# Performance work log

Measured on AMD Instinct MI355X. Metric: run time of the kernel, lower is better.

Reference implementation:

```python
import jax, jax.numpy as jnp
import numpy as np
from jax import lax

B, C, T = 16, 32, 512
GAF_SIZE = 128
LATENT = 128
EPS = 1e-8


def _conv(x, w, b, stride):
    # x: (N, Cin, H, W), w: (Cout, Cin, kh, kw)
    y = lax.conv_general_dilated(x, w, (stride, stride), 'SAME',
                                 dimension_numbers=('NCHW', 'OIHW', 'NCHW'))
    return jax.nn.relu(y + b[None, :, None, None])


def _compute_gaf(x_raw):
    # x_raw: (B, C, T) -> (B*C, 2, S, S) with channels [GASF, GADF]
    S = GAF_SIZE
    # Piecewise Aggregate Approximation: T -> S
    x = x_raw.reshape(B, C, S, T // S).mean(axis=-1)        # (B, C, S)
    # Min-max normalize each series to [-1, 1]
    mn = x.min(axis=-1, keepdims=True)
    mx = x.max(axis=-1, keepdims=True)
    x = jnp.clip(2.0 * (x - mn) / (mx - mn + EPS) - 1.0, -1.0, 1.0)
    # phi = arccos(x); use trig identities to avoid explicit arccos
    sq = jnp.sqrt(jnp.clip(1.0 - x * x, 0.0, 1.0))          # sin(phi)
    xi, xj = x[..., :, None], x[..., None, :]
    si, sj = sq[..., :, None], sq[..., None, :]
    gasf = xi * xj - si * sj                                 # cos(phi_i + phi_j)
    gadf = si * xj - xi * sj                                 # sin(phi_i - phi_j)
    gaf = jnp.stack([gasf, gadf], axis=2)                    # (B, C, 2, S, S)
    return gaf.reshape(B * C, 2, S, S).astype(jnp.float32)


def _encoder(gaf, W1, b1, W2, b2, W3, b3, W4, b4, Wfc, bfc):
    h = _conv(gaf, W1, b1, 2)   # (B*C, 32, 64, 64)
    h = _conv(h, W2, b2, 2)     # (B*C, 64, 32, 32)
    h = _conv(h, W3, b3, 2)     # (B*C, 128, 16, 16)
    h = _conv(h, W4, b4, 2)     # (B*C, 256, 8, 8)
    h = h.mean(axis=(2, 3))     # global average pool -> (B*C, 256)
    return h @ Wfc + bfc        # (B*C, LATENT)


def setup_inputs() -> dict:
    key = jax.random.key(0)
    ks = jax.random.split(key, 12)
    p = lambda k, shp: (jax.random.normal(k, shp, dtype=jnp.float32) * 0.05)
    return {
        'x_raw': jax.random.normal(ks[0], (B, C, T), dtype=jnp.float32),
        'W1': p(ks[1], (32, 2, 3, 3)),   'b1': jnp.zeros((32,), jnp.float32),
        'W2': p(ks[2], (64, 32, 3, 3)),  'b2': jnp.zeros((64,), jnp.float32),
        'W3': p(ks[3], (128, 64, 3, 3)), 'b3': jnp.zeros((128,), jnp.float32),
        'W4': p(ks[4], (256, 128, 3, 3)),'b4': jnp.zeros((256,), jnp.float32),
        'Wfc': p(ks[5], (256, LATENT)),  'bfc': jnp.zeros((LATENT,), jnp.float32),
    }


def reference(x_raw, W1, b1, W2, b2, W3, b3, W4, b4, Wfc, bfc):
    # GAF computed from detached raw EEG in the original (numpy CPU path)
    gaf = lax.stop_gradient(_compute_gaf(x_raw))
    z = _encoder(gaf, W1, b1, W2, b2, W3, b3, W4, b4, Wfc, bfc)
    return z.reshape(B, C, LATENT).mean(axis=1)              # (B, LATENT)
```

## Files before the change

### kernel.cpp

```cpp
#include <hip/hip_runtime.h>
#include <hip/hip_bf16.h>

#define DEV __device__ __forceinline__

constexpr int kB = 16, kC = 32, kT = 512, kS = 128, kBC = 512, kLatent = 128;
constexpr float kEps = 1e-8f;

using bf16 = __hip_bfloat16;
using bf16x8 = __attribute__((ext_vector_type(8))) short;
using f32x4  = __attribute__((ext_vector_type(4))) float;

DEV unsigned short f2bf(float v) {
    bf16 h = __float2bfloat16(v);
    return *(unsigned short*)&h;
}

DEV void gld16(const void* g, void* l) {
    __builtin_amdgcn_global_load_lds(
        (const __attribute__((address_space(1))) unsigned*)g,
        (__attribute__((address_space(3))) unsigned*)l, 16, 0, 0);
}

__global__ void gaf_stats_kernel(const float* __restrict__ x_raw,
                                 float* __restrict__ xn, float* __restrict__ sq) {
    int bc = blockIdx.x;
    int s  = threadIdx.x;
    const float* xp = x_raw + (size_t)bc * kT;
    float v = 0.25f * (xp[4*s] + xp[4*s+1] + xp[4*s+2] + xp[4*s+3]);
    __shared__ float smn[kS], smx[kS];
    smn[s] = v; smx[s] = v;
    __syncthreads();
    for (int off = kS/2; off > 0; off >>= 1) {
        if (s < off) {
            smn[s] = fminf(smn[s], smn[s+off]);
            smx[s] = fmaxf(smx[s], smx[s+off]);
        }
        __syncthreads();
    }
    float mn = smn[0], mx = smx[0];
    float xv = 2.0f * (v - mn) / (mx - mn + kEps) - 1.0f;
    xv = fminf(fmaxf(xv, -1.0f), 1.0f);
    float sv = sqrtf(fminf(fmaxf(1.0f - xv*xv, 0.0f), 1.0f));
    xn[bc*kS + s] = xv;
    sq[bc*kS + s] = sv;
}

__global__ void wtrans_all_kernel(const float* __restrict__ w1,
                                  const float* __restrict__ w2,
                                  const float* __restrict__ w3,
                                  const float* __restrict__ w4,
                                  bf16* __restrict__ w1b, bf16* __restrict__ wt2,
                                  bf16* __restrict__ wt3, bf16* __restrict__ wt4) {
    int idx = blockIdx.x * blockDim.x + threadIdx.x;
    if (idx < 1024) {
        int oc = idx >> 5, k = idx & 31;
        w1b[idx] = __float2bfloat16(k < 18 ? w1[oc*18 + k] : 0.0f);
        return;
    }
    idx -= 1024;
    const float* src; bf16* dst; int CIN, COUT;
    if (idx < 18432)       { src = w2; dst = wt2; CIN = 32;  COUT = 64;  }
    else if (idx < 92160)  { idx -= 18432;  src = w3; dst = wt3; CIN = 64;  COUT = 128; }
    else if (idx < 387072) { idx -= 92160;  src = w4; dst = wt4; CIN = 128; COUT = 256; }
    else return;
    int ic = idx % CIN;
    int oc = (idx / CIN) % COUT;
    int t  = idx / (CIN * COUT);
    dst[((size_t)t * COUT + oc) * CIN + ic] = __float2bfloat16(src[((size_t)oc * CIN + ic) * 9 + t]);
}

__global__ __launch_bounds__(256, 2)
void conv12_kernel(const float* __restrict__ xn, const float* __restrict__ sq,
                   const bf16* __restrict__ w1b, const float* __restrict__ b1,
                   const bf16* __restrict__ wt2, const float* __restrict__ b2,
                   bf16* __restrict__ out, int img0) {
    __shared__ float xl[kS], sl[kS];
    __shared__ __align__(16) union { short G[576][40]; short H[2][288][40]; } U;
    __shared__ __align__(16) short Bs2[3][64][32];
    __shared__ __align__(16) short W1s[32][40];

    int tid  = threadIdx.x;
    int lane = tid & 63;
    int wv   = tid >> 6;
    int mblk = blockIdx.x;
    int bz   = blockIdx.y;
    int bc   = img0 + bz;

    gld16((const char*)wt2 + 0*4096 + tid*16, (char*)Bs2 + 0*4096 + tid*16);
    gld16((const char*)wt2 + 1*4096 + tid*16, (char*)Bs2 + 1*4096 + tid*16);

    if (tid < 128) {
        xl[tid] = xn[(size_t)bc * kS + tid];
        int rr = tid >> 2, sg = tid & 3;
        *(uint4*)&W1s[rr][sg*8] = *(const uint4*)(w1b + rr*32 + sg*8);
    } else {
        sl[tid - 128] = sq[(size_t)bc * kS + (tid - 128)];
    }
    __syncthreads();

    #pragma unroll
    for (int it = 0; it < 3; ++it) {
        int idx = it * 256 + tid;
        if (idx >= 576) break;
        int trow = idx >> 6, hx = idx & 63;
        int iy = 8 * mblk + trow;
        unsigned int pk[16];
        #pragma unroll
        for (int j = 0; j < 16; ++j) pk[j] = 0u;
        if (iy < 64) {
            float xr[3], sr[3], xc[3], sc[3];
            #pragma unroll
            for (int k = 0; k < 3; ++k) {
                int iyy = 2*iy + k, ixx = 2*hx + k;
                bool vy = iyy < kS, vx = ixx < kS;
                xr[k] = vy ? xl[iyy] : 0.0f;  sr[k] = vy ? sl[iyy] : 0.0f;
                xc[k] = vx ? xl[ixx] : 0.0f;  sc[k] = vx ? sl[ixx] : 0.0f;
            }
            unsigned short gs[18];
            #pragma unroll
            for (int ky = 0; ky < 3; ++ky)
                #pragma unroll
                for (int kx = 0; kx < 3; ++kx) {
                    gs[ky*3+kx]   = f2bf(xr[ky]*xc[kx] - sr[ky]*sc[kx]);
                    gs[9+ky*3+kx] = f2bf(sr[ky]*xc[kx] - xr[ky]*sc[kx]);
                }
            #pragma unroll
            for (int j = 0; j < 9; ++j)
                pk[j] = (unsigned int)gs[2*j] | ((unsigned int)gs[2*j+1] << 16);
        }
        #pragma unroll
        for (int j = 0; j < 4; ++j) *(uint4*)&U.G[idx][j*8] = ((uint4*)pk)[j];
    }
    __syncthreads();

    f32x4 c1[9][2];
    bf16x8 w1f0 = *(const bf16x8*)&W1s[(lane & 15)][(lane>>4)*8];
    bf16x8 w1f1 = *(const bf16x8*)&W1s[16 + (lane & 15)][(lane>>4)*8];
    #pragma unroll
    for (int j = 0; j < 9; ++j) {
        int mt = 4*j + wv;
        bf16x8 af = *(const bf16x8*)&U.G[mt*16 + (lane & 15)][(lane>>4)*8];
        f32x4 zz = f32x4{0.f, 0.f, 0.f, 0.f};
        c1[j][0] = __builtin_amdgcn_mfma_f32_16x16x32_bf16(af, w1f0, zz, 0, 0, 0);
        c1[j][1] = __builtin_amdgcn_mfma_f32_16x16x32_bf16(af, w1f1, zz, 0, 0, 0);
    }
    __syncthreads();

    #pragma unroll
    for (int j = 0; j < 9; ++j) {
        int mt = 4*j + wv;
        #pragma unroll
        for (int h = 0; h < 2; ++h) {
            int oc = h*16 + (lane & 15);
            float bb = b1[oc];
            #pragma unroll
            for (int rg = 0; rg < 4; ++rg) {
                int pos = mt*16 + (lane>>4)*4 + rg;
                int trow = pos >> 6, hx = pos & 63;
                float v = fmaxf(c1[j][h][rg] + bb, 0.0f);
                if (8*mblk + trow >= 64) v = 0.0f;
                U.H[hx & 1][trow*32 + (hx >> 1)][oc] = (short)f2bf(v);
            }
        }
    }
    __syncthreads();

    f32x4 acc[2][4];
    #pragma unroll
    for (int i = 0; i < 2; ++i)
        #pragma unroll
        for (int j = 0; j < 4; ++j) acc[i][j] = f32x4{0.f, 0.f, 0.f, 0.f};

    for (int tap = 0; tap < 9; ++tap) {
        if (tap + 2 < 9)
            gld16((const char*)wt2 + (tap+2)*4096 + tid*16,
                  (char*)Bs2 + ((tap+2)%3)*4096 + tid*16);
        int ky = tap / 3, kx = tap % 3;
        int trow = 2*wv + ky;
        const short* bsl = &Bs2[tap%3][0][0];
        bf16x8 af[2], bfr[4];
        #pragma unroll
        for (int mi = 0; mi < 2; ++mi) {
            int ocol = mi*16 + (lane & 15);
            int x = 2*ocol + kx;
            bf16x8 z = {0,0,0,0,0,0,0,0};
            af[mi] = (x < 64) ? *(const bf16x8*)&U.H[kx & 1][trow*32 + (x>>1)][(lane>>4)*8] : z;
        }
        #pragma unroll
        for (int ni = 0; ni < 4; ++ni)
            bfr[ni] = *(const bf16x8*)&bsl[(ni*16 + (lane&15))*32 + (lane>>4)*8];
        #pragma unroll
        for (int mi = 0; mi < 2; ++mi)
            #pragma unroll
            for (int ni = 0; ni < 4; ++ni)
                acc[mi][ni] = __builtin_amdgcn_mfma_f32_16x16x32_bf16(af[mi], bfr[ni], acc[mi][ni], 0, 0, 0);
        __syncthreads();
    }

    int oy = 4*mblk + wv;
    #pragma unroll
    for (int ni = 0; ni < 4; ++ni) {
        int oc = ni*16 + (lane & 15);
        float b = b2[oc];
        #pragma unroll
        for (int mi = 0; mi < 2; ++mi)
            #pragma unroll
            for (int rg = 0; rg < 4; ++rg) {
                int ocol = 16*mi + (lane>>4)*4 + rg;
                float v = fmaxf(acc[mi][ni][rg] + b, 0.0f);
                out[(((size_t)bz*32 + oy)*32 + ocol)*64 + oc] = __float2bfloat16(v);
            }
    }
}

__global__ __launch_bounds__(256)
void conv34_kernel(const bf16* __restrict__ h2, const bf16* __restrict__ wt3,
                   const float* __restrict__ b3, const bf16* __restrict__ wt4,
                   const float* __restrict__ b4, float* __restrict__ pooled,
                   int img0, const bf16* __restrict__ zbuf) {
    __shared__ __align__(16) short H3[257*128];
    __shared__ __align__(16) short stA[2*256*32];
    __shared__ __align__(16) short stB[2*128*32];

    int tid  = threadIdx.x;
    int lane = tid & 63;
    int wv   = tid >> 6;
    int img  = blockIdx.x;

    if (tid < 128) H3[256*128 + tid] = 0;

    auto issue1 = [&](int s, int buf) {
        int tap = s >> 1, icb = (s & 1) * 32;
        int ky = tap / 3, kx = tap % 3;
        #pragma unroll
        for (int j = 0; j < 4; ++j) {
            int row = wv*64 + j*16 + (lane >> 2);
            int oy = row >> 4, ox = row & 15;
            int iy = 2*oy + ky, ix = 2*ox + kx;
            const bf16* src = (iy < 32 && ix < 32)
                ? h2 + (((size_t)img*32 + iy)*32 + ix)*64 + icb + (lane & 3)*8
                : zbuf + (lane & 3)*8;
            gld16(src, (char*)&stA[buf*8192 + (wv*64 + j*16)*32] + lane*16);
        }
        #pragma unroll
        for (int j = 0; j < 2; ++j) {
            int brow = wv*32 + j*16 + (lane >> 2);
            const bf16* src = wt3 + ((size_t)tap*128 + brow)*64 + icb + (lane & 3)*8;
            gld16(src, (char*)&stB[buf*4096 + (wv*32 + j*16)*32] + lane*16);
        }
    };

    f32x4 acc[4][8];
    #pragma unroll
    for (int i = 0; i < 4; ++i)
        #pragma unroll
        for (int j = 0; j < 8; ++j) acc[i][j] = f32x4{0.f, 0.f, 0.f, 0.f};

    issue1(0, 0);
    __syncthreads();

    for (int s = 0; s < 18; ++s) {
        int cur = s & 1;
        if (s + 1 < 18) issue1(s + 1, cur ^ 1);
        bf16x8 af[4];
        #pragma unroll
        for (int mi = 0; mi < 4; ++mi)
            af[mi] = *(const bf16x8*)&stA[cur*8192 + (wv*64 + mi*16 + (lane&15))*32 + (lane>>4)*8];
        #pragma unroll
        for (int ni = 0; ni < 8; ++ni) {
            bf16x8 bfr = *(const bf16x8*)&stB[cur*4096 + (ni*16 + (lane&15))*32 + (lane>>4)*8];
            #pragma unroll
            for (int mi = 0; mi < 4; ++mi)
                acc[mi][ni] = __builtin_amdgcn_mfma_f32_16x16x32_bf16(af[mi], bfr, acc[mi][ni], 0, 0, 0);
        }
        __syncthreads();
    }

    #pragma unroll
    for (int ni = 0; ni < 8; ++ni) {
        int oc = ni*16 + (lane & 15);
        float bb = b3[oc];
        int q = oc >> 3, ql = oc & 7;
        #pragma unroll
        for (int mi = 0; mi < 4; ++mi)
            #pragma unroll
            for (int rg = 0; rg < 4; ++rg) {
                int pos = wv*64 + mi*16 + (lane>>4)*4 + rg;
                float v = fmaxf(acc[mi][ni][rg] + bb, 0.0f);
                H3[pos*128 + (q ^ ((pos>>1)&7))*8 + ql] = (short)f2bf(v);
            }
    }

    auto issue2 = [&](int s, int buf) {
        int tap = s >> 2, icb = (s & 3) * 32;
        #pragma unroll
        for (int j = 0; j < 4; ++j) {
            int brow = wv*64 + j*16 + (lane >> 2);
            const bf16* src = wt4 + ((size_t)tap*256 + brow)*128 + icb + (lane & 3)*8;
            gld16(src, (char*)&stA[buf*8192 + (wv*64 + j*16)*32] + lane*16);
        }
    };

    issue2(0, 0);
    __syncthreads();

    f32x4 ac4[4][4];
    #pragma unroll
    for (int i = 0; i < 4; ++i)
        #pragma unroll
        for (int j = 0; j < 4; ++j) ac4[i][j] = f32x4{0.f, 0.f, 0.f, 0.f};

    for (int s = 0; s < 36; ++s) {
        int cur = s & 1;
        if (s + 1 < 36) issue2(s + 1, cur ^ 1);
        int tap = s >> 2, kq0 = (s & 3) * 4 + (lane >> 4);
        int ky = tap / 3, kx = tap % 3;
        bf16x8 af[4];
        #pragma unroll
        for (int mi = 0; mi < 4; ++mi) {
            int m = mi*16 + (lane & 15);
            int oy = m >> 3, ox = m & 7;
            int iy = 2*oy + ky, ix = 2*ox + kx;
            int pos = (iy < 16 && ix < 16) ? iy*16 + ix : 256;
            af[mi] = *(const bf16x8*)&H3[pos*128 + (kq0 ^ ((pos>>1)&7))*8];
        }
        #pragma unroll
        for (int ni = 0; ni < 4; ++ni) {
            bf16x8 bfr = *(const bf16x8*)&stA[cur*8192 + (wv*64 + ni*16 + (lane&15))*32 + (lane>>4)*8];
            #pragma unroll
            for (int mi = 0; mi < 4; ++mi)
                ac4[mi][ni] = __builtin_amdgcn_mfma_f32_16x16x32_bf16(af[mi], bfr, ac4[mi][ni], 0, 0, 0);
        }
        __syncthreads();
    }

    #pragma unroll
    for (int ni = 0; ni < 4; ++ni) {
        int oc = wv*64 + ni*16 + (lane & 15);
        float bb = b4[oc];
        float ssum = 0.0f;
        #pragma unroll
        for (int mi = 0; mi < 4; ++mi)
            #pragma unroll
            for (int rg = 0; rg < 4; ++rg) ssum += fmaxf(ac4[mi][ni][rg] + bb, 0.0f);
        ssum += __shfl_xor(ssum, 16);
        ssum += __shfl_xor(ssum, 32);
        if (lane < 16)
            pooled[((size_t)(img0 + img))*256 + wv*64 + ni*16 + lane] = ssum * (1.0f/64.0f);
    }
}

__global__ void poolfc_kernel(const float* __restrict__ pooled, const float* __restrict__ Wfc,
                              const float* __restrict__ bfc, float* __restrict__ out) {
    int b = blockIdx.x;
    int t = threadIdx.x;
    __shared__ float pm[256];
    #pragma unroll
    for (int q = 0; q < 2; ++q) {
        int k = q*128 + t;
        float s = 0.0f;
        #pragma unroll
        for (int c = 0; c < kC; ++c) s += pooled[((size_t)(b*kC + c))*256 + k];
        pm[k] = s * (1.0f/kC);
    }
    __syncthreads();
    float acc = bfc[t];
    for (int k = 0; k < 256; ++k) acc = fmaf(pm[k], Wfc[(size_t)k*kLatent + t], acc);
    out[(size_t)b*kLatent + t] = acc;
}

extern "C" void kernel_launch(void* const* d_in, const int* in_sizes, int n_in,
                              void* d_out, int out_size, void* d_ws, size_t ws_size,
                              hipStream_t stream) {
    const float* x_raw = (const float*)d_in[0];
    const float* W1 = (const float*)d_in[1];  const float* b1 = (const float*)d_in[2];
    const float* W2 = (const float*)d_in[3];  const float* b2 = (const float*)d_in[4];
    const float* W3 = (const float*)d_in[5];  const float* b3 = (const float*)d_in[6];
    const float* W4 = (const float*)d_in[7];  const float* b4 = (const float*)d_in[8];
    const float* Wfc = (const float*)d_in[9]; const float* bfc = (const float*)d_in[10];
    float* out = (float*)d_out;

    char* wsb = (char*)d_ws;
    float* xn     = (float*)(wsb);
    float* sq     = (float*)(wsb + (256u<<10));
    float* pooled = (float*)(wsb + (512u<<10));
    bf16* Wt2     = (bf16*)(wsb + (1280u<<10));
    bf16* Wt3     = (bf16*)(wsb + (1316u<<10));
    bf16* Wt4     = (bf16*)(wsb + (1460u<<10));
    bf16* W1b     = (bf16*)(wsb + (2036u<<10));
    bf16* zbuf    = (bf16*)(wsb + (2040u<<10));
    char* chunk_base = wsb + (2048u<<10);

    const size_t perImg = 32u*32u*64u*2u;
    int chunk = 4;
    for (int c = 512; c >= 4; c >>= 1) {
        if ((2048u<<10) + (size_t)c * perImg <= ws_size) { chunk = c; break; }
    }

    hipMemsetAsync(zbuf, 0, 1024, stream);
    gaf_stats_kernel<<<kBC, kS, 0, stream>>>(x_raw, xn, sq);
    wtrans_all_kernel<<<(388096 + 255)/256, 256, 0, stream>>>(W1, W2, W3, W4, W1b, Wt2, Wt3, Wt4);

    for (int img0 = 0; img0 < kBC; img0 += chunk) {
        int nimg = chunk;
        bf16* h2 = (bf16*)chunk_base;

        conv12_kernel<<<dim3(8, nimg), 256, 0, stream>>>(xn, sq, W1b, b1, Wt2, b2, h2, img0);
        conv34_kernel<<<nimg, 256, 0, stream>>>(h2, Wt3, b3, Wt4, b4, pooled, img0, zbuf);
    }

    poolfc_kernel<<<kB, kLatent, 0, stream>>>(pooled, Wfc, bfc, out);
}
```

Before: 244.4 us.

## Split fused conv3/conv4 kernel into separate kernels with global h3 buffer

Replaces the single per-image conv3+conv4 kernel with two kernels: conv3 runs two blocks per image (each covering half the output rows) and writes a swizzled, parity-split h3 to global memory, and conv4 loads that h3 into LDS. Conv3 now stages the whole input half-tile in LDS once and register-prefetches weights instead of async double-buffered im2col loads. This raises parallelism and occupancy (launch bounds 2 blocks/SM, smaller LDS per block) at the cost of an extra global round trip for h3 and an additional kernel launch per chunk.

```diff
diff --git a/kernel.cpp b/kernel.cpp
--- a/kernel.cpp
+++ b/kernel.cpp
@@ -213,140 +213,192 @@
     }
 }
 
-__global__ __launch_bounds__(256)
-void conv34_kernel(const bf16* __restrict__ h2, const bf16* __restrict__ wt3,
-                   const float* __restrict__ b3, const bf16* __restrict__ wt4,
-                   const float* __restrict__ b4, float* __restrict__ pooled,
-                   int img0, const bf16* __restrict__ zbuf) {
-    __shared__ __align__(16) short H3[257*128];
-    __shared__ __align__(16) short stA[2*256*32];
-    __shared__ __align__(16) short stB[2*128*32];
+__global__ __launch_bounds__(256, 2)
+void conv3_kernel(const bf16* __restrict__ h2, const bf16* __restrict__ wt3,
+                  const float* __restrict__ b3, bf16* __restrict__ h3g) {
+    __shared__ __align__(16) short T[34816];
+    __shared__ __align__(16) short Bs[4096];
 
     int tid  = threadIdx.x;
     int lane = tid & 63;
     int wv   = tid >> 6;
+    int half = blockIdx.x;
+    int img  = blockIdx.y;
+    const bf16* h2i = h2 + (size_t)img * 65536;
+
+    for (int it = 0; it < 17; ++it) {
+        int o = it*256 + tid;
+        int r = o >> 8, c = o & 255;
+        int ix = c >> 3, icq = c & 7;
+        int gr = half*16 + r;
+        uint4 v = {0u,0u,0u,0u};
+        if (gr < 32) v = *(const uint4*)(h2i + gr*2048 + ix*64 + icq*8);
+        int dst = ((((ix&1)*17 + r)*16 + (ix>>1))*8 + (icq ^ ((ix>>1)&7)))*8;
+        *(uint4*)&T[dst] = v;
+    }
+    int brow = tid >> 1, bseg = tid & 1;
+    {
+        const bf16* p = wt3 + (size_t)brow*64 + bseg*16;
+        uint4 v0 = *(const uint4*)p, v1 = *(const uint4*)(p + 8);
+        *(uint4*)&Bs[brow*32 + bseg*16]     = v0;
+        *(uint4*)&Bs[brow*32 + bseg*16 + 8] = v1;
+    }
+    __syncthreads();
+
+    f32x4 acc[2][8];
+    #pragma unroll
+    for (int i = 0; i < 2; ++i)
+        #pragma unroll
+        for (int j = 0; j < 8; ++j) acc[i][j] = f32x4{0.f,0.f,0.f,0.f};
+
+    for (int s = 0; s < 18; ++s) {
+        uint4 nb0, nb1;
+        if (s + 1 < 18) {
+            int tapn = (s+1) >> 1, icbn = ((s+1) & 1) * 32;
+            const bf16* p = wt3 + ((size_t)tapn*128 + brow)*64 + icbn + bseg*16;
+            nb0 = *(const uint4*)p; nb1 = *(const uint4*)(p + 8);
+        }
+        int tap = s >> 1, icq0 = (s & 1) * 4;
+        int ky = tap / 3, kx = tap % 3;
+        bf16x8 af[2], bfr[8];
+        #pragma unroll
+        for (int mi = 0; mi < 2; ++mi) {
+            int m = wv*32 + mi*16 + (lane & 15);
+            int oyL = m >> 4, ox3 = m & 15;
+            int iy = 2*oyL + ky, ix = 2*ox3 + kx;
+            int par = ix & 1, colx = ix >> 1;
+            int colc = colx > 15 ? 15 : colx;
+            int addr = (((par*17 + iy)*16 + colc)*8 + ((icq0 + (lane>>4)) ^ (colc & 7)))*8;
+            bf16x8 v = *(const bf16x8*)&T[addr];
+            bf16x8 z = {0,0,0,0,0,0,0,0};
+            af[mi] = (ix < 32) ? v : z;
+        }
+        #pragma unroll
+        for (int ni = 0; ni < 8; ++ni)
+            bfr[ni] = *(const bf16x8*)&Bs[(ni*16 + (lane&15))*32 + (lane>>4)*8];
+        #pragma unroll
+        for (int mi = 0; mi < 2; ++mi)
+            #pragma unroll
+            for (int ni = 0; ni < 8; ++ni)
+                acc[mi][ni] = __builtin_amdgcn_mfma_f32_16x16x32_bf16(af[mi], bfr[ni], acc[mi][ni], 0, 0, 0);
+        __syncthreads();
+        if (s + 1 < 18) {
+            *(uint4*)&Bs[brow*32 + bseg*16]     = nb0;
+            *(uint4*)&Bs[brow*32 + bseg*16 + 8] = nb1;
+            __syncthreads();
+        }
+    }
+
+    bf16* h3o = h3g + (size_t)img * 32768;
+    #pragma unroll
+    for (int ni = 0; ni < 8; ++ni) {
+        int oc3 = ni*16 + (lane & 15);
+        float bb = b3[oc3];
+        int kq = oc3 >> 3, ql = oc3 & 7;
+        #pragma unroll
+        for (int mi = 0; mi < 2; ++mi)
+            #pragma unroll
+            for (int rg = 0; rg < 4; ++rg) {
+                int m = wv*32 + mi*16 + (lane>>4)*4 + rg;
+                int oyL = m >> 4, ox3 = m & 15;
+                int iy4 = half*8 + oyL;
+                int par = ox3 & 1, col4 = ox3 >> 1;
+                int slot = kq ^ col4;
+                int off = ((par*16 + iy4)*8 + col4)*128 + slot*8 + ql;
+                float v = fmaxf(acc[mi][ni][rg] + bb, 0.0f);
+                h3o[off] = __float2bfloat16(v);
+            }
+    }
+}
+
+__global__ __launch_bounds__(256, 2)
+void conv4_kernel(const bf16* __restrict__ h3g, const bf16* __restrict__ wt4,
+                  const float* __restrict__ b4, float* __restrict__ pooled,
+                  int img0) {
+    __shared__ __align__(16) short H3s[32768];
+    __shared__ __align__(16) short Bs[8192];
+
+    int tid  = threadIdx.x;
+    int lane = tid & 63;
+    int wn   = tid >> 6;
     int img  = blockIdx.x;
 
-    if (tid < 128) H3[256*128 + tid] = 0;
-
-    auto issue1 = [&](int s, int buf) {
-        int tap = s >> 1, icb = (s & 1) * 32;
+    const char* h3b = (const char*)(h3g + (size_t)img * 32768);
+    #pragma unroll
+    for (int it = 0; it < 16; ++it)
+        gld16(h3b + (it*256 + tid)*16, (char*)H3s + (it*256 + tid)*16);
+
+    uint4 vb[4];
+    {
+        const bf16* p = wt4 + (size_t)tid * 128;
+        #pragma unroll
+        for (int j = 0; j < 4; ++j) vb[j] = *(const uint4*)(p + j*8);
+        #pragma unroll
+        for (int j = 0; j < 4; ++j) *(uint4*)&Bs[tid*32 + j*8] = vb[j];
+    }
+    __syncthreads();
+
+    f32x4 acc[4][4];
+    #pragma unroll
+    for (int i = 0; i < 4; ++i)
+        #pragma unroll
+        for (int j = 0; j < 4; ++j) acc[i][j] = f32x4{0.f,0.f,0.f,0.f};
+
+    for (int s = 0; s < 36; ++s) {
+        uint4 nb[4];
+        if (s + 1 < 36) {
+            int tapn = (s+1) >> 2, icbn = ((s+1) & 3) * 32;
+            const bf16* p = wt4 + ((size_t)tapn*256 + tid)*128 + icbn;
+            #pragma unroll
+            for (int j = 0; j < 4; ++j) nb[j] = *(const uint4*)(p + j*8);
+        }
+        int tap = s >> 2;
         int ky = tap / 3, kx = tap % 3;
-        #pragma unroll
-        for (int j = 0; j < 4; ++j) {
-            int row = wv*64 + j*16 + (lane >> 2);
-            int oy = row >> 4, ox = row & 15;
-            int iy = 2*oy + ky, ix = 2*ox + kx;
-            const bf16* src = (iy < 32 && ix < 32)
-                ? h2 + (((size_t)img*32 + iy)*32 + ix)*64 + icb + (lane & 3)*8
-                : zbuf + (lane & 3)*8;
-            gld16(src, (char*)&stA[buf*8192 + (wv*64 + j*16)*32] + lane*16);
-        }
-        #pragma unroll
-        for (int j = 0; j < 2; ++j) {
-            int brow = wv*32 + j*16 + (lane >> 2);
-            const bf16* src = wt3 + ((size_t)tap*128 + brow)*64 + icb + (lane & 3)*8;
-            gld16(src, (char*)&stB[buf*4096 + (wv*32 + j*16)*32] + lane*16);
-        }
-    };
-
-    f32x4 acc[4][8];
-    #pragma unroll
-    for (int i = 0; i < 4; ++i)
-        #pragma unroll
-        for (int j = 0; j < 8; ++j) acc[i][j] = f32x4{0.f, 0.f, 0.f, 0.f};
-
-    issue1(0, 0);
-    __syncthreads();
-
-    for (int s = 0; s < 18; ++s) {
-        int cur = s & 1;
-        if (s + 1 < 18) issue1(s + 1, cur ^ 1);
-        bf16x8 af[4];
-        #pragma unroll
-        for (int mi = 0; mi < 4; ++mi)
-            af[mi] = *(const bf16x8*)&stA[cur*8192 + (wv*64 + mi*16 + (lane&15))*32 + (lane>>4)*8];
-        #pragma unroll
-        for (int ni = 0; ni < 8; ++ni) {
-            bf16x8 bfr = *(const bf16x8*)&stB[cur*4096 + (ni*16 + (lane&15))*32 + (lane>>4)*8];
-            #pragma unroll
-            for (int mi = 0; mi < 4; ++mi)
-                acc[mi][ni] = __builtin_amdgcn_mfma_f32_16x16x32_bf16(af[mi], bfr, acc[mi][ni], 0, 0, 0);
-        }
-        __syncthreads();
-    }
-
-    #pragma unroll
-    for (int ni = 0; ni < 8; ++ni) {
-        int oc = ni*16 + (lane & 15);
-        float bb = b3[oc];
-        int q = oc >> 3, ql = oc & 7;
-        #pragma unroll
-        for (int mi = 0; mi < 4; ++mi)
-            #pragma unroll
-            for (int rg = 0; rg < 4; ++rg) {
-                int pos = wv*64 + mi*16 + (lane>>4)*4 + rg;
-                float v = fmaxf(acc[mi][ni][rg] + bb, 0.0f);
-                H3[pos*128 + (q ^ ((pos>>1)&7))*8 + ql] = (short)f2bf(v);
-            }
-    }
-
-    auto issue2 = [&](int s, int buf) {
-        int tap = s >> 2, icb = (s & 3) * 32;
-        #pragma unroll
-        for (int j = 0; j < 4; ++j) {
-            int brow = wv*64 + j*16 + (lane >> 2);
-            const bf16* src = wt4 + ((size_t)tap*256 + brow)*128 + icb + (lane & 3)*8;
-            gld16(src, (char*)&stA[buf*8192 + (wv*64 + j*16)*32] + lane*16);
-        }
-    };
-
-    issue2(0, 0);
-    __syncthreads();
-
-    f32x4 ac4[4][4];
-    #pragma unroll
-    for (int i = 0; i < 4; ++i)
-        #pragma unroll
-        for (int j = 0; j < 4; ++j) ac4[i][j] = f32x4{0.f, 0.f, 0.f, 0.f};
-
-    for (int s = 0; s < 36; ++s) {
-        int cur = s & 1;
-        if (s + 1 < 36) issue2(s + 1, cur ^ 1);
-        int tap = s >> 2, kq0 = (s & 3) * 4 + (lane >> 4);
-        int ky = tap / 3, kx = tap % 3;
-        bf16x8 af[4];
+        int kq0 = (s & 3)*4 + (lane >> 4);
+        bf16x8 af[4], bfr[4];
         #pragma unroll
         for (int mi = 0; mi < 4; ++mi) {
             int m = mi*16 + (lane & 15);
             int oy = m >> 3, ox = m & 7;
             int iy = 2*oy + ky, ix = 2*ox + kx;
-            int pos = (iy < 16 && ix < 16) ? iy*16 + ix : 256;
-            af[mi] = *(const bf16x8*)&H3[pos*128 + (kq0 ^ ((pos>>1)&7))*8];
-        }
-        #pragma unroll
-        for (int ni = 0; ni < 4; ++ni) {
-            bf16x8 bfr = *(const bf16x8*)&stA[cur*8192 + (wv*64 + ni*16 + (lane&15))*32 + (lane>>4)*8];
-            #pragma unroll
-            for (int mi = 0; mi < 4; ++mi)
-                ac4[mi][ni] = __builtin_amdgcn_mfma_f32_16x16x32_bf16(af[mi], bfr, ac4[mi][ni], 0, 0, 0);
-        }
+            bool valid = (iy < 16) && (ix < 16);
+            int iyc = iy > 15 ? 15 : iy, ixc = ix > 15 ? 15 : ix;
+            int par = ixc & 1, col = ixc >> 1;
+            int slot = kq0 ^ col;
+            int addr = ((par*16 + iyc)*8 + col)*128 + slot*8;
+            bf16x8 v = *(const bf16x8*)&H3s[addr];
+            bf16x8 z = {0,0,0,0,0,0,0,0};
+            af[mi] = valid ? v : z;
+        }
+        #pragma unroll
+        for (int ni = 0; ni < 4; ++ni)
+            bfr[ni] = *(const bf16x8*)&Bs[(wn*64 + ni*16 + (lane&15))*32 + (lane>>4)*8];
+        #pragma unroll
+        for (int mi = 0; mi < 4; ++mi)
+            #pragma unroll
+            for (int ni = 0; ni < 4; ++ni)
+                acc[mi][ni] = __builtin_amdgcn_mfma_f32_16x16x32_bf16(af[mi], bfr[ni], acc[mi][ni], 0, 0, 0);
         __syncthreads();
+        if (s + 1 < 36) {
+            #pragma unroll
+            for (int j = 0; j < 4; ++j) *(uint4*)&Bs[tid*32 + j*8] = nb[j];
+            __syncthreads();
+        }
     }
 
     #pragma unroll
     for (int ni = 0; ni < 4; ++ni) {
-        int oc = wv*64 + ni*16 + (lane & 15);
+        int oc = wn*64 + ni*16 + (lane & 15);
         float bb = b4[oc];
         float ssum = 0.0f;
         #pragma unroll
         for (int mi = 0; mi < 4; ++mi)
             #pragma unroll
-            for (int rg = 0; rg < 4; ++rg) ssum += fmaxf(ac4[mi][ni][rg] + bb, 0.0f);
+            for (int rg = 0; rg < 4; ++rg) ssum += fmaxf(acc[mi][ni][rg] + bb, 0.0f);
         ssum += __shfl_xor(ssum, 16);
         ssum += __shfl_xor(ssum, 32);
         if (lane < 16)
-            pooled[((size_t)(img0 + img))*256 + wv*64 + ni*16 + lane] = ssum * (1.0f/64.0f);
+            pooled[((size_t)(img0 + img))*256 + oc] = ssum * (1.0f/64.0f);
     }
 }
 
@@ -388,25 +440,26 @@
     bf16* Wt3     = (bf16*)(wsb + (1316u<<10));
     bf16* Wt4     = (bf16*)(wsb + (1460u<<10));
     bf16* W1b     = (bf16*)(wsb + (2036u<<10));
-    bf16* zbuf    = (bf16*)(wsb + (2040u<<10));
     char* chunk_base = wsb + (2048u<<10);
 
-    const size_t perImg = 32u*32u*64u*2u;
+    const size_t perH2 = 32u*32u*64u*2u, perH3 = 64u<<10;
+    const size_t perImg = perH2 + perH3;
     int chunk = 4;
     for (int c = 512; c >= 4; c >>= 1) {
         if ((2048u<<10) + (size_t)c * perImg <= ws_size) { chunk = c; break; }
     }
 
-    hipMemsetAsync(zbuf, 0, 1024, stream);
     gaf_stats_kernel<<<kBC, kS, 0, stream>>>(x_raw, xn, sq);
     wtrans_all_kernel<<<(388096 + 255)/256, 256, 0, stream>>>(W1, W2, W3, W4, W1b, Wt2, Wt3, Wt4);
 
     for (int img0 = 0; img0 < kBC; img0 += chunk) {
         int nimg = chunk;
-        bf16* h2 = (bf16*)chunk_base;
+        bf16* h2  = (bf16*)chunk_base;
+        bf16* h3g = (bf16*)(chunk_base + (size_t)chunk * perH2);
 
         conv12_kernel<<<dim3(8, nimg), 256, 0, stream>>>(xn, sq, W1b, b1, Wt2, b2, h2, img0);
-        conv34_kernel<<<nimg, 256, 0, stream>>>(h2, Wt3, b3, Wt4, b4, pooled, img0, zbuf);
+        conv3_kernel<<<dim3(2, nimg), 256, 0, stream>>>(h2, Wt3, b3, h3g);
+        conv4_kernel<<<nimg, 256, 0, stream>>>(h3g, Wt4, b4, pooled, img0);
     }
 
     poolfc_kernel<<<kB, kLatent, 0, stream>>>(pooled, Wfc, bfc, out);
```

New measurement: 282.3 us. 15.5% more time.
